# Kernel tuning notes

Hardware: AMD Instinct MI355X
Metric: run time of the kernel (lower is better)

## Reference

```python
import jax, jax.numpy as jnp
import numpy as np

# Model dims (GatedAttentionLayer of Qwen3.5 ANE hybrid stack)
C = 2048      # hidden_size
H = 16        # num_attention_heads
HK = 4        # num_key_value_heads
D = 128       # head_dim
ROT = 32      # rotary_dim = head_dim * partial_rotary_factor (0.25)
S = 1024      # sequence length (prefill)
CTX = 1024    # kv cache context length
N_ATTN = 6    # number of full-attention layers -> kv_cache leading dim 2*N_ATTN
EPS = 1e-6
ROPE_THETA = 1e7


def _rotate_half(x):
    h = x.shape[-1] // 2
    return jnp.concatenate([-x[..., h:], x[..., :h]], axis=-1)


def _rms_norm(x, w, eps=EPS):
    # Qwen3.5 convention: stored weight is (w - 1), applied as (1 + weight)
    r = jax.lax.rsqrt(jnp.mean(x * x, axis=-1, keepdims=True) + eps)
    return x * r * (1.0 + w)


def setup_inputs() -> dict:
    key = jax.random.key(0)
    ks = jax.random.split(key, 6)
    hidden_states = jax.random.normal(ks[0], (1, C, 1, S), jnp.float32)
    q_proj_w = jax.random.normal(ks[1], (H * 2 * D, C), jnp.float32) * 0.02  # q + gate
    k_proj_w = jax.random.normal(ks[2], (HK * D, C), jnp.float32) * 0.02
    v_proj_w = jax.random.normal(ks[3], (HK * D, C), jnp.float32) * 0.02
    o_proj_w = jax.random.normal(ks[4], (C, H * D), jnp.float32) * 0.02
    q_norm_w = jnp.zeros((D,), jnp.float32)
    k_norm_w = jnp.zeros((D,), jnp.float32)
    kv_cache = jnp.zeros((2 * N_ATTN, HK, CTX, D), jnp.float32)
    position_ids = jnp.arange(S, dtype=jnp.int32)
    # causal mask: 0 on/below diagonal, -1e9 above
    causal_mask = jnp.where(
        jnp.arange(CTX)[None, :] <= jnp.arange(S)[:, None], 0.0, -1e9
    ).astype(jnp.float32)[None, None]  # [1,1,S,CTX]
    # RoPE tables over rotary_dim
    inv_freq = 1.0 / (ROPE_THETA ** (jnp.arange(0, ROT, 2, dtype=jnp.float32) / ROT))
    t = jnp.arange(CTX, dtype=jnp.float32)
    freqs = jnp.outer(t, inv_freq)          # [CTX, ROT//2]
    emb = jnp.concatenate([freqs, freqs], -1)  # [CTX, ROT]
    cos_cached = jnp.cos(emb)
    sin_cached = jnp.sin(emb)
    return dict(hidden_states=hidden_states, q_proj_w=q_proj_w, k_proj_w=k_proj_w,
                v_proj_w=v_proj_w, o_proj_w=o_proj_w, q_norm_w=q_norm_w,
                k_norm_w=k_norm_w, kv_cache=kv_cache, causal_mask=causal_mask,
                position_ids=position_ids, cos_cached=cos_cached,
                sin_cached=sin_cached, attn_layer_idx=0)


def reference(hidden_states, q_proj_w, k_proj_w, v_proj_w, o_proj_w,
              q_norm_w, k_norm_w, kv_cache, causal_mask, position_ids,
              cos_cached, sin_cached, attn_layer_idx):
    x = hidden_states[0, :, 0, :]                     # [C, S]
    q_raw = q_proj_w @ x                              # [H*2D, S]  (1x1 Conv2d == GEMM)
    qg = q_raw.reshape(H, 2 * D, S)
    q = jnp.transpose(qg[:, :D, :], (0, 2, 1))        # [H, S, D]
    gate = jnp.transpose(qg[:, D:, :], (0, 2, 1))     # [H, S, D]
    k = jnp.transpose((k_proj_w @ x).reshape(HK, D, S), (0, 2, 1))  # [HK, S, D]
    v = jnp.transpose((v_proj_w @ x).reshape(HK, D, S), (0, 2, 1))  # [HK, S, D]

    q = _rms_norm(q, q_norm_w)
    k = _rms_norm(k, k_norm_w)

    cos = cos_cached[position_ids]   # [S, ROT]
    sin = sin_cached[position_ids]

    def rope(t):
        rot, pas = t[..., :ROT], t[..., ROT:]
        rot = rot * cos + _rotate_half(rot) * sin
        return jnp.concatenate([rot, pas], axis=-1)

    q, k = rope(q), rope(k)

    # prefill cache write at pos_start = position_ids[0]
    k_idx = 2 * attn_layer_idx
    v_idx = k_idx + 1
    pos_start = position_ids[0]
    kv_cache = jax.lax.dynamic_update_slice(kv_cache, k[None], (k_idx, 0, pos_start, 0))
    kv_cache = jax.lax.dynamic_update_slice(kv_cache, v[None], (v_idx, 0, pos_start, 0))

    g = H // HK  # GQA repeat (expand+reshape == contiguous repeat)
    k_full = jnp.repeat(kv_cache[k_idx], g, axis=0)   # [H, CTX, D]
    v_full = jnp.repeat(kv_cache[v_idx], g, axis=0)   # [H, CTX, D]

    scale = D ** -0.5
    attn = jnp.einsum('hsd,htd->hst', q, k_full) * scale + causal_mask[0]
    attn = jax.nn.softmax(attn, axis=-1)
    out = jnp.einsum('hst,htd->hsd', attn, v_full)    # [H, S, D]
    out = out * jax.nn.sigmoid(gate)
    out = jnp.transpose(out, (0, 2, 1)).reshape(H * D, S)
    output = (o_proj_w @ out)[None, :, None, :]       # [1, C, 1, S]
    return output
```

## Files before the change

### kernel.cpp

```cpp
#include <hip/hip_runtime.h>
#include <cstdint>

#define S_LEN 1024
#define C_DIM 2048
#define NH    16
#define NHK   4
#define HD    128
#define ROT   32
#define SCALE 0.08838834764831845f

typedef __bf16 bf16x8 __attribute__((ext_vector_type(8)));
typedef float floatx4 __attribute__((ext_vector_type(4)));
typedef float floatx16 __attribute__((ext_vector_type(16)));
typedef unsigned short ushortx8 __attribute__((ext_vector_type(8)));

__device__ __forceinline__ unsigned short f2bf(float f) {
  union { float f; uint32_t u; } x; x.f = f;
  uint32_t r = (x.u + 0x7fffu + ((x.u >> 16) & 1u)) >> 16;
  return (unsigned short)r;
}
__device__ __forceinline__ float bf2f(unsigned short v) {
  union { uint32_t u; float f; } x; x.u = (uint32_t)v << 16; return x.f;
}

__device__ __forceinline__ void async_copy16(const unsigned short* g, unsigned short* l) {
  __builtin_amdgcn_global_load_lds(
      (const __attribute__((address_space(1))) void*)g,
      (__attribute__((address_space(3))) void*)l,
      16, 0, 0);
}

__device__ __forceinline__ void bar_lds_only() {
  asm volatile("s_waitcnt lgkmcnt(0)" ::: "memory");
  __builtin_amdgcn_s_barrier();
}

__device__ __forceinline__ int swz8(int row) { return (row ^ (row >> 3)) & 7; }

__global__ __launch_bounds__(256)
void prep_kernel(const float* __restrict__ qw, const float* __restrict__ kw,
                 const float* __restrict__ vw, const float* __restrict__ ow,
                 unsigned short* __restrict__ wout,
                 const float* __restrict__ x, unsigned short* __restrict__ xT) {
  __shared__ float t[32][33];
  int bid = blockIdx.x;
  if (bid < 14336) {
    const int NQ = 4096 * 2048 / 4, NK = 512 * 2048 / 4, NV = 512 * 2048 / 4;
    int i = bid * 256 + threadIdx.x;
    const float* src; int j;
    if (i < NQ) { src = qw; j = i; }
    else if (i < NQ + NK) { src = kw; j = i - NQ; }
    else if (i < NQ + NK + NV) { src = vw; j = i - NQ - NK; }
    else { src = ow; j = i - NQ - NK - NV; }
    float4 v = ((const float4*)src)[j];
    ushort4 o;
    o.x = f2bf(v.x); o.y = f2bf(v.y); o.z = f2bf(v.z); o.w = f2bf(v.w);
    ((ushort4*)wout)[i] = o;
  } else {
    int b2 = bid - 14336;
    int st = b2 & 31, ct = b2 >> 5;
    int c = threadIdx.x & 31, rq = threadIdx.x >> 5;
#pragma unroll
    for (int i = 0; i < 4; ++i) {
      int r = rq + i * 8;
      t[r][c] = x[(size_t)(ct * 32 + r) * S_LEN + st * 32 + c];
    }
    __syncthreads();
#pragma unroll
    for (int i = 0; i < 4; ++i) {
      int r = rq + i * 8;
      xT[(size_t)(st * 32 + r) * C_DIM + ct * 32 + c] = f2bf(t[c][r]);
    }
  }
}

__device__ __forceinline__ void norm_rope_epi512(
    floatx16& acc, float (*pp)[32],
    const float* __restrict__ w, const int* __restrict__ pos_ids,
    const float* __restrict__ cosc, const float* __restrict__ sinc,
    unsigned short* __restrict__ outp,
    int wave, int lane, int wm, int scol0) {
  int l31 = lane & 31, half = lane >> 5;
  float s = 0.f;
#pragma unroll
  for (int reg = 0; reg < 16; ++reg) { float v = acc[reg]; s += v * v; }
  s += __shfl_xor(s, 32);
  if (half == 0) pp[wave][l31] = s;
  __syncthreads();
  int gb = wave & 4;
  float tot = pp[gb][l31] + pp[gb + 1][l31] + pp[gb + 2][l31] + pp[gb + 3][l31];
  float rn = rsqrtf(tot * (1.0f / 128.0f) + 1e-6f);
  int scol = scol0 + l31;
  int pos = pos_ids[scol];
  bool rope = (wm == 0);
#pragma unroll
  for (int g = 0; g < 4; ++g) {
    int dbase = wm + half * 4 + g * 8;
    ushort4 o;
#pragma unroll
    for (int rr = 0; rr < 4; ++rr) {
      int reg = g * 4 + rr;
      int d = dbase + rr;
      float v = acc[reg] * rn * (1.0f + w[d]);
      if (rope) {
        float cv = cosc[pos * ROT + d], sv = sinc[pos * ROT + d];
        int d2 = (d < 16) ? d + 16 : d - 16;
        float pv = acc[reg ^ 8] * rn * (1.0f + w[d2]);
        v = v * cv + ((d < 16) ? -pv : pv) * sv;
      }
      ((unsigned short*)&o)[rr] = f2bf(v);
    }
    *(ushort4*)&outp[(size_t)scol * HD + dbase] = o;
  }
}

#define GEMM512_CORE(EXTRA_LB)                                                     \
  int tid = threadIdx.x, wave = tid >> 6, lane = tid & 63;                         \
  int l31 = lane & 31, half = lane >> 5;                                           \
  int wm = (wave & 3) * 32, wn = (wave >> 2) * 32;                                 \
  int m0 = blockIdx.x * 128, n0 = blockIdx.y * 64;                                 \
  int r8 = tid >> 3, c8 = tid & 7;                                                 \
  int arow1 = r8 + 64;                                                             \
  int apos0 = c8 ^ swz8(r8), apos1 = c8 ^ swz8(arow1), bpos = apos0;               \
  int aswz = swz8(wm + l31), bswz = swz8(wn + l31);                                \
  const unsigned short* Ag = A + (size_t)m0 * C_DIM;                               \
  const unsigned short* Bg = BT + (size_t)n0 * C_DIM;                              \
  floatx16 acc = (floatx16)0.f;                                                    \
  ushortx8 rA0, rA1, rB;                                                           \
  rA0 = *(const ushortx8*)(Ag + (size_t)r8 * C_DIM + c8 * 8);                      \
  rA1 = *(const ushortx8*)(Ag + (size_t)arow1 * C_DIM + c8 * 8);                   \
  rB  = *(const ushortx8*)(Bg + (size_t)r8 * C_DIM + c8 * 8);                      \
  *(ushortx8*)&Asm[0][r8 * 64 + apos0 * 8] = rA0;                                  \
  *(ushortx8*)&Asm[0][arow1 * 64 + apos1 * 8] = rA1;                               \
  *(ushortx8*)&Bsm[0][r8 * 64 + bpos * 8] = rB;                                    \
  bar_lds_only();                                                                  \
  for (int t = 0; t < 32; ++t) {                                                   \
    int b = t & 1;                                                                 \
    if (t < 31) {                                                                  \
      int kt = (t + 1) * 64;                                                       \
      rA0 = *(const ushortx8*)(Ag + (size_t)r8 * C_DIM + kt + c8 * 8);             \
      rA1 = *(const ushortx8*)(Ag + (size_t)arow1 * C_DIM + kt + c8 * 8);          \
      rB  = *(const ushortx8*)(Bg + (size_t)r8 * C_DIM + kt + c8 * 8);             \
    }                                                                              \
    _Pragma("unroll")                                                              \
    for (int kb = 0; kb < 4; ++kb) {                                               \
      int ca = (((kb << 1) | half) ^ aswz) << 3;                                   \
      int cb = (((kb << 1) | half) ^ bswz) << 3;                                   \
      bf16x8 av = *(const bf16x8*)&Asm[b][(wm + l31) * 64 + ca];                   \
      bf16x8 bv = *(const bf16x8*)&Bsm[b][(wn + l31) * 64 + cb];                   \
      acc = __builtin_amdgcn_mfma_f32_32x32x16_bf16(av, bv, acc, 0, 0, 0);         \
    }                                                                              \
    if (t < 31) {                                                                  \
      *(ushortx8*)&Asm[b ^ 1][r8 * 64 + apos0 * 8] = rA0;                          \
      *(ushortx8*)&Asm[b ^ 1][arow1 * 64 + apos1 * 8] = rA1;                       \
      *(ushortx8*)&Bsm[b ^ 1][r8 * 64 + bpos * 8] = rB;                            \
    }                                                                              \
    bar_lds_only();                                                                \
  }

__global__ __launch_bounds__(512, 6)
void gemm_qkv_fused(const unsigned short* __restrict__ A,
                    const unsigned short* __restrict__ BT,
                    const float* __restrict__ qw, const float* __restrict__ kw,
                    const int* __restrict__ pos_ids,
                    const float* __restrict__ cosc, const float* __restrict__ sinc,
                    unsigned short* __restrict__ qb, unsigned short* __restrict__ kbuf,
                    unsigned short* __restrict__ vTb, unsigned short* __restrict__ sgb) {
  __shared__ unsigned short Asm[2][128 * 64];
  __shared__ unsigned short Bsm[2][64 * 64];
  __shared__ float pp[8][32];
  GEMM512_CORE()

  int scol0 = n0 + wn;
  int ty = blockIdx.x;
  if (ty < 32) {
    int h = ty >> 1;
    if ((ty & 1) == 0) {
      norm_rope_epi512(acc, pp, qw, pos_ids, cosc, sinc,
                       qb + (size_t)h * S_LEN * HD, wave, lane, wm, scol0);
    } else {
      int scol = scol0 + l31;
#pragma unroll
      for (int g = 0; g < 4; ++g) {
        int dbase = wm + half * 4 + g * 8;
        ushort4 o;
#pragma unroll
        for (int rr = 0; rr < 4; ++rr)
          ((unsigned short*)&o)[rr] = f2bf(1.0f / (1.0f + __expf(-acc[g * 4 + rr])));
        *(ushort4*)&sgb[((size_t)h * S_LEN + scol) * HD + dbase] = o;
      }
    }
  } else if (ty < 36) {
    int hk = ty - 32;
    norm_rope_epi512(acc, pp, kw, pos_ids, cosc, sinc,
                     kbuf + (size_t)hk * S_LEN * HD, wave, lane, wm, scol0);
  } else {
    int hk = ty - 36;
#pragma unroll
    for (int reg = 0; reg < 16; ++reg) {
      int d = wm + (reg & 3) + 8 * (reg >> 2) + 4 * half;
      vTb[(size_t)hk * HD * S_LEN + (size_t)d * S_LEN + scol0 + l31] = f2bf(acc[reg]);
    }
  }
}

__global__ __launch_bounds__(512, 6)
void gemm_oproj(const unsigned short* __restrict__ A,
                const unsigned short* __restrict__ BT,
                float* __restrict__ C) {
  __shared__ unsigned short Asm[2][128 * 64];
  __shared__ unsigned short Bsm[2][64 * 64];
  GEMM512_CORE()

#pragma unroll
  for (int reg = 0; reg < 16; ++reg) {
    int row = m0 + wm + (reg & 3) + 8 * (reg >> 2) + 4 * half;
    C[(size_t)row * S_LEN + n0 + wn + l31] = acc[reg];
  }
}

__global__ __launch_bounds__(256)
void attn_kernel(const unsigned short* __restrict__ qb,
                 const unsigned short* __restrict__ kbuf,
                 const unsigned short* __restrict__ vTb,
                 float* __restrict__ pm, float* __restrict__ pl,
                 float* __restrict__ pO0, float* __restrict__ pO1) {
  __shared__ __align__(16) unsigned short Ks[64 * 128];
  __shared__ __align__(16) unsigned short Vs[128 * 64];
  __shared__ __align__(16) unsigned short Ps[4][16][72];
  int h = blockIdx.x, qt = blockIdx.y, ch = blockIdx.z;
  int t0 = ch * 4;
  if (t0 > qt) return;
  int t1 = min(qt, t0 + 3);
  int s0 = qt * 64;
  int hk = h >> 2;
  int tid = threadIdx.x, wave = tid >> 6, lane = tid & 63;
  int l16 = lane & 15, quad = lane >> 4;
  int lsw = l16 & 7;

  const unsigned short* qg = qb + ((size_t)(h * S_LEN + s0 + wave * 16 + l16)) * HD;
  bf16x8 qfr[4];
#pragma unroll
  for (int kb = 0; kb < 4; ++kb)
    qfr[kb] = *(const bf16x8*)(qg + kb * 32 + quad * 8);

  float m_r[4], l_r[4];
#pragma unroll
  for (int r = 0; r < 4; ++r) { m_r[r] = -1e30f; l_r[r] = 0.f; }
  floatx4 acc_o[8];
#pragma unroll
  for (int i = 0; i < 8; ++i) acc_o[i] = (floatx4)0.f;
  int srow_base = s0 + wave * 16 + quad * 4;

  const unsigned short* kg0 = kbuf + (size_t)hk * S_LEN * HD;
  const unsigned short* vg0 = vTb + (size_t)hk * HD * S_LEN;

  int kr4 = lane >> 4, kc16 = lane & 15;
  int vr8 = lane >> 3, vc8 = lane & 7;

  for (int t = t0; t <= t1; ++t) {
    int jt = t * 64;
#pragma unroll
    for (int i = 0; i < 4; ++i) {
      int rbase = wave * 16 + i * 4;
      int row = rbase + kr4;
      int cs = kc16 ^ (row & 7);
      async_copy16(kg0 + (size_t)(jt + row) * HD + cs * 8, Ks + rbase * 128);
    }
#pragma unroll
    for (int i = 0; i < 4; ++i) {
      int rbase = wave * 32 + i * 8;
      int row = rbase + vr8;
      int cs = vc8 ^ (row & 7);
      async_copy16(vg0 + (size_t)row * S_LEN + jt + cs * 8, Vs + rbase * 64);
    }
    __syncthreads();

    floatx4 acc_s[4];
#pragma unroll
    for (int ni = 0; ni < 4; ++ni) acc_s[ni] = (floatx4)0.f;
#pragma unroll
    for (int kb = 0; kb < 4; ++kb) {
#pragma unroll
      for (int ni = 0; ni < 4; ++ni) {
        int cl = (kb * 4 + quad) ^ lsw;
        bf16x8 bk = *(const bf16x8*)&Ks[(ni * 16 + l16) * 128 + cl * 8];
        acc_s[ni] = __builtin_amdgcn_mfma_f32_16x16x32_bf16(qfr[kb], bk, acc_s[ni], 0, 0, 0);
      }
    }

    bool diag = (t == qt);
    float alpha[4];
#pragma unroll
    for (int r = 0; r < 4; ++r) {
      float scv[4];
      float mx = -1e30f;
#pragma unroll
      for (int ni = 0; ni < 4; ++ni) {
        float sv = acc_s[ni][r] * SCALE;
        if (diag) {
          int jg = jt + ni * 16 + l16;
          if (jg > srow_base + r) sv = -1e30f;
        }
        scv[ni] = sv;
        mx = fmaxf(mx, sv);
      }
#pragma unroll
      for (int off = 8; off; off >>= 1) mx = fmaxf(mx, __shfl_xor(mx, off, 16));
      float mnew = fmaxf(m_r[r], mx);
      float psv = 0.f;
#pragma unroll
      for (int ni = 0; ni < 4; ++ni) {
        float pv = (scv[ni] > -1e29f) ? __expf(scv[ni] - mnew) : 0.f;
        Ps[wave][quad * 4 + r][ni * 16 + l16] = f2bf(pv);
        psv += pv;
      }
#pragma unroll
      for (int off = 8; off; off >>= 1) psv += __shfl_xor(psv, off, 16);
      alpha[r] = __expf(m_r[r] - mnew);
      m_r[r] = mnew;
      l_r[r] = l_r[r] * alpha[r] + psv;
    }
#pragma unroll
    for (int i = 0; i < 8; ++i)
#pragma unroll
      for (int r = 0; r < 4; ++r) acc_o[i][r] *= alpha[r];
    __threadfence_block();

#pragma unroll
    for (int kb2 = 0; kb2 < 2; ++kb2) {
      bf16x8 ap = *(const bf16x8*)&Ps[wave][l16][kb2 * 32 + quad * 8];
#pragma unroll
      for (int ni2 = 0; ni2 < 8; ++ni2) {
        int cl = (kb2 * 4 + quad) ^ lsw;
        bf16x8 bv = *(const bf16x8*)&Vs[(ni2 * 16 + l16) * 64 + cl * 8];
        acc_o[ni2] = __builtin_amdgcn_mfma_f32_16x16x32_bf16(ap, bv, acc_o[ni2], 0, 0, 0);
      }
    }
    __syncthreads();
  }

  size_t pmbase = ((size_t)(h * 16 + qt) * 4 + ch) * 64;
  float* pOp = (ch < 2) ? pO0 + ((size_t)(h * 16 + qt) * 2 + ch) * 8192
                        : pO1 + ((size_t)(h * 16 + qt) * 2 + (ch - 2)) * 8192;
#pragma unroll
  for (int r = 0; r < 4; ++r) {
    int rrow = wave * 16 + quad * 4 + r;
    if (l16 == 0) { pm[pmbase + rrow] = m_r[r]; pl[pmbase + rrow] = l_r[r]; }
#pragma unroll
    for (int ni2 = 0; ni2 < 8; ++ni2)
      pOp[rrow * 128 + ni2 * 16 + l16] = acc_o[ni2][r];
  }
}

__global__ __launch_bounds__(256)
void attn_merge(const float* __restrict__ pm, const float* __restrict__ pl,
                const float* __restrict__ pO0, const float* __restrict__ pO1,
                const unsigned short* __restrict__ sgb,
                unsigned short* __restrict__ outT) {
  int h = blockIdx.x, qt = blockIdx.y;
  int vc = (qt >> 2) + 1;
  size_t base = (size_t)(h * 16 + qt) * 4;
  int lane32 = threadIdx.x & 31, rb = threadIdx.x >> 5;
  int d = lane32 * 4;
#pragma unroll
  for (int rr = 0; rr < 8; ++rr) {
    int row = rr * 8 + rb;
    float M = -1e30f;
    for (int c = 0; c < vc; ++c) M = fmaxf(M, pm[(base + c) * 64 + row]);
    float L = 0.f;
    floatx4 acc = (floatx4)0.f;
    for (int c = 0; c < vc; ++c) {
      float w = __expf(pm[(base + c) * 64 + row] - M);
      L += w * pl[(base + c) * 64 + row];
      const float* Op = (c < 2) ? pO0 + ((size_t)(h * 16 + qt) * 2 + c) * 8192
                                : pO1 + ((size_t)(h * 16 + qt) * 2 + (c - 2)) * 8192;
      floatx4 o = *(const floatx4*)&Op[row * 128 + d];
#pragma unroll
      for (int j = 0; j < 4; ++j) acc[j] += w * o[j];
    }
    float inv = 1.0f / L;
    int s = qt * 64 + row;
    ushort4 sg4 = *(const ushort4*)&sgb[((size_t)h * S_LEN + s) * HD + d];
    ushort4 out4;
#pragma unroll
    for (int j = 0; j < 4; ++j)
      ((unsigned short*)&out4)[j] = f2bf(acc[j] * inv * bf2f(((unsigned short*)&sg4)[j]));
    *(ushort4*)&outT[(size_t)s * (NH * HD) + h * HD + d] = out4;
  }
}

extern "C" void kernel_launch(void* const* d_in, const int* in_sizes, int n_in,
                              void* d_out, int out_size, void* d_ws, size_t ws_size,
                              hipStream_t stream) {
  const float* hs       = (const float*)d_in[0];
  const float* q_proj_w = (const float*)d_in[1];
  const float* k_proj_w = (const float*)d_in[2];
  const float* v_proj_w = (const float*)d_in[3];
  const float* o_proj_w = (const float*)d_in[4];
  const float* q_norm_w = (const float*)d_in[5];
  const float* k_norm_w = (const float*)d_in[6];
  const int*   pos_ids  = (const int*)d_in[9];
  const float* cos_c    = (const float*)d_in[10];
  const float* sin_c    = (const float*)d_in[11];
  float* out = (float*)d_out;

  char* ws = (char*)d_ws;
  unsigned short* wqkv = (unsigned short*)(ws + 0);
  unsigned short* wo   = (unsigned short*)(ws + 20971520);
  unsigned short* xT   = (unsigned short*)(ws + 29360128);
  unsigned short* qb   = (unsigned short*)(ws + 33554432);
  unsigned short* kbuf = (unsigned short*)(ws + 37748736);
  unsigned short* vTb  = (unsigned short*)(ws + 38797312);
  unsigned short* sgb  = (unsigned short*)(ws + 39845888);
  unsigned short* aoT  = (unsigned short*)(ws + 44040192);
  float*          pO0  = (float*)(ws + 0);
  float*          pO1  = (float*)(ws + 48234496);
  float*          pm   = (float*)(ws + 65011712);
  float*          pl   = (float*)(ws + 65273856);

  prep_kernel<<<14336 + 2048, 256, 0, stream>>>(q_proj_w, k_proj_w, v_proj_w, o_proj_w,
                                                wqkv, hs, xT);
  gemm_qkv_fused<<<dim3(40, 16), 512, 0, stream>>>(wqkv, xT, q_norm_w, k_norm_w,
                                                   pos_ids, cos_c, sin_c,
                                                   qb, kbuf, vTb, sgb);
  attn_kernel<<<dim3(16, 16, 4), 256, 0, stream>>>(qb, kbuf, vTb, pm, pl, pO0, pO1);
  attn_merge<<<dim3(16, 16), 256, 0, stream>>>(pm, pl, pO0, pO1, sgb, aoT);
  gemm_oproj<<<dim3(16, 16), 512, 0, stream>>>(wo, aoT, out);
}
```

Baseline: 241.8 us.

## Rewrite QKV GEMM with 4 waves, direct global-to-LDS async loads

The fused QKV projection GEMM moves from 8 waves (512 threads) holding one 32x32 accumulator each to 4 waves holding two accumulators, so each A fragment read from LDS feeds two MFMAs. Tile staging now uses global_load_lds async copies into double-buffered LDS, gated by vmcnt waits, instead of staging through registers and LDS stores. The RMS-norm/RoPE epilogue is reworked to handle two column blocks per wave. The intent is to cut LDS traffic and register staging overhead and overlap loads with compute, at the cost of fewer waves per block for hiding latency.

Result: faster. 232.7 us (-3.8%).

```diff
diff --git a/kernel.cpp b/kernel.cpp
--- a/kernel.cpp
+++ b/kernel.cpp
@@ -29,6 +29,8 @@
       (__attribute__((address_space(3))) void*)l,
       16, 0, 0);
 }
+
+#define WAIT_VM(N) asm volatile("s_waitcnt vmcnt(" #N ")" ::: "memory")
 
 __device__ __forceinline__ void bar_lds_only() {
   asm volatile("s_waitcnt lgkmcnt(0)" ::: "memory");
@@ -74,43 +76,145 @@
   }
 }
 
-__device__ __forceinline__ void norm_rope_epi512(
-    floatx16& acc, float (*pp)[32],
+__device__ __forceinline__ void norm_rope_epi4(
+    floatx16 (&acc)[2], float (*pp)[64],
     const float* __restrict__ w, const int* __restrict__ pos_ids,
     const float* __restrict__ cosc, const float* __restrict__ sinc,
     unsigned short* __restrict__ outp,
     int wave, int lane, int wm, int scol0) {
   int l31 = lane & 31, half = lane >> 5;
-  float s = 0.f;
-#pragma unroll
-  for (int reg = 0; reg < 16; ++reg) { float v = acc[reg]; s += v * v; }
-  s += __shfl_xor(s, 32);
-  if (half == 0) pp[wave][l31] = s;
+#pragma unroll
+  for (int ni = 0; ni < 2; ++ni) {
+    float s = 0.f;
+#pragma unroll
+    for (int reg = 0; reg < 16; ++reg) { float v = acc[ni][reg]; s += v * v; }
+    s += __shfl_xor(s, 32);
+    if (half == 0) pp[wave][ni * 32 + l31] = s;
+  }
   __syncthreads();
-  int gb = wave & 4;
-  float tot = pp[gb][l31] + pp[gb + 1][l31] + pp[gb + 2][l31] + pp[gb + 3][l31];
-  float rn = rsqrtf(tot * (1.0f / 128.0f) + 1e-6f);
-  int scol = scol0 + l31;
-  int pos = pos_ids[scol];
-  bool rope = (wm == 0);
-#pragma unroll
-  for (int g = 0; g < 4; ++g) {
-    int dbase = wm + half * 4 + g * 8;
-    ushort4 o;
-#pragma unroll
-    for (int rr = 0; rr < 4; ++rr) {
-      int reg = g * 4 + rr;
-      int d = dbase + rr;
-      float v = acc[reg] * rn * (1.0f + w[d]);
-      if (rope) {
-        float cv = cosc[pos * ROT + d], sv = sinc[pos * ROT + d];
-        int d2 = (d < 16) ? d + 16 : d - 16;
-        float pv = acc[reg ^ 8] * rn * (1.0f + w[d2]);
-        v = v * cv + ((d < 16) ? -pv : pv) * sv;
-      }
-      ((unsigned short*)&o)[rr] = f2bf(v);
-    }
-    *(ushort4*)&outp[(size_t)scol * HD + dbase] = o;
+#pragma unroll
+  for (int ni = 0; ni < 2; ++ni) {
+    int ci = ni * 32 + l31;
+    float tot = pp[0][ci] + pp[1][ci] + pp[2][ci] + pp[3][ci];
+    float rn = rsqrtf(tot * (1.0f / 128.0f) + 1e-6f);
+    int scol = scol0 + ni * 32 + l31;
+    int pos = pos_ids[scol];
+    bool rope = (wm == 0);
+#pragma unroll
+    for (int g = 0; g < 4; ++g) {
+      int dbase = wm + half * 4 + g * 8;
+      ushort4 o;
+#pragma unroll
+      for (int rr = 0; rr < 4; ++rr) {
+        int reg = g * 4 + rr;
+        int d = dbase + rr;
+        float v = acc[ni][reg] * rn * (1.0f + w[d]);
+        if (rope) {
+          float cv = cosc[pos * ROT + d], sv = sinc[pos * ROT + d];
+          int d2 = (d < 16) ? d + 16 : d - 16;
+          float pv = acc[ni][reg ^ 8] * rn * (1.0f + w[d2]);
+          v = v * cv + ((d < 16) ? -pv : pv) * sv;
+        }
+        ((unsigned short*)&o)[rr] = f2bf(v);
+      }
+      *(ushort4*)&outp[(size_t)scol * HD + dbase] = o;
+    }
+  }
+}
+
+#define STAGE_QKV4(B_, KT)                                                     \
+  { _Pragma("unroll")                                                          \
+    for (int i = 0; i < 4; ++i) {                                              \
+      int row = wm + i * 8 + sr;                                               \
+      async_copy16(Ag + (size_t)row * C_DIM + (KT) + (sc ^ swz8(row)) * 8,     \
+                   &Asm[B_][(wm + i * 8) * 64]);                               \
+    }                                                                          \
+    _Pragma("unroll")                                                          \
+    for (int i = 0; i < 2; ++i) {                                              \
+      int row = wave * 16 + i * 8 + sr;                                        \
+      async_copy16(Bg + (size_t)row * C_DIM + (KT) + (sc ^ swz8(row)) * 8,     \
+                   &Bsm[B_][(wave * 16 + i * 8) * 64]);                        \
+    } }
+
+__global__ __launch_bounds__(256, 3)
+void gemm_qkv_fused(const unsigned short* __restrict__ A,
+                    const unsigned short* __restrict__ BT,
+                    const float* __restrict__ qw, const float* __restrict__ kw,
+                    const int* __restrict__ pos_ids,
+                    const float* __restrict__ cosc, const float* __restrict__ sinc,
+                    unsigned short* __restrict__ qb, unsigned short* __restrict__ kbuf,
+                    unsigned short* __restrict__ vTb, unsigned short* __restrict__ sgb) {
+  __shared__ unsigned short Asm[2][128 * 64];
+  __shared__ unsigned short Bsm[2][64 * 64];
+  __shared__ float pp[4][64];
+  int tid = threadIdx.x, wave = tid >> 6, lane = tid & 63;
+  int l31 = lane & 31, half = lane >> 5;
+  int wm = wave * 32;
+  int m0 = blockIdx.x * 128, n0 = blockIdx.y * 64;
+  int sr = lane >> 3, sc = lane & 7;
+  const unsigned short* Ag = A + (size_t)m0 * C_DIM;
+  const unsigned short* Bg = BT + (size_t)n0 * C_DIM;
+  int aswz = swz8(wm + l31);
+  int bswz0 = swz8(l31), bswz1 = swz8(32 + l31);
+  floatx16 acc[2];
+  acc[0] = (floatx16)0.f; acc[1] = (floatx16)0.f;
+
+  STAGE_QKV4(0, 0)
+  STAGE_QKV4(1, 64)
+
+  for (int t = 0; t < 32; ++t) {
+    int b = t & 1;
+    if (t < 31) { WAIT_VM(6); } else { WAIT_VM(0); }
+    __builtin_amdgcn_s_barrier();
+#pragma unroll
+    for (int kb = 0; kb < 4; ++kb) {
+      int c2 = (kb << 1) | half;
+      bf16x8 av  = *(const bf16x8*)&Asm[b][(wm + l31) * 64 + ((c2 ^ aswz) << 3)];
+      bf16x8 b0v = *(const bf16x8*)&Bsm[b][l31 * 64 + ((c2 ^ bswz0) << 3)];
+      bf16x8 b1v = *(const bf16x8*)&Bsm[b][(32 + l31) * 64 + ((c2 ^ bswz1) << 3)];
+      acc[0] = __builtin_amdgcn_mfma_f32_32x32x16_bf16(av, b0v, acc[0], 0, 0, 0);
+      acc[1] = __builtin_amdgcn_mfma_f32_32x32x16_bf16(av, b1v, acc[1], 0, 0, 0);
+    }
+    bar_lds_only();
+    if (t < 30) STAGE_QKV4(b, (t + 2) * 64)
+  }
+
+  int scol0 = n0;
+  int ty = blockIdx.x;
+  if (ty < 32) {
+    int h = ty >> 1;
+    if ((ty & 1) == 0) {
+      norm_rope_epi4(acc, pp, qw, pos_ids, cosc, sinc,
+                     qb + (size_t)h * S_LEN * HD, wave, lane, wm, scol0);
+    } else {
+#pragma unroll
+      for (int ni = 0; ni < 2; ++ni) {
+        int scol = scol0 + ni * 32 + l31;
+#pragma unroll
+        for (int g = 0; g < 4; ++g) {
+          int dbase = wm + half * 4 + g * 8;
+          ushort4 o;
+#pragma unroll
+          for (int rr = 0; rr < 4; ++rr)
+            ((unsigned short*)&o)[rr] = f2bf(1.0f / (1.0f + __expf(-acc[ni][g * 4 + rr])));
+          *(ushort4*)&sgb[((size_t)h * S_LEN + scol) * HD + dbase] = o;
+        }
+      }
+    }
+  } else if (ty < 36) {
+    int hk = ty - 32;
+    norm_rope_epi4(acc, pp, kw, pos_ids, cosc, sinc,
+                   kbuf + (size_t)hk * S_LEN * HD, wave, lane, wm, scol0);
+  } else {
+    int hk = ty - 36;
+#pragma unroll
+    for (int ni = 0; ni < 2; ++ni)
+#pragma unroll
+      for (int reg = 0; reg < 16; ++reg) {
+        int d = wm + (reg & 3) + 8 * (reg >> 2) + 4 * half;
+        vTb[(size_t)hk * HD * S_LEN + (size_t)d * S_LEN + scol0 + ni * 32 + l31] =
+            f2bf(acc[ni][reg]);
+      }
   }
 }
 
@@ -159,52 +263,6 @@
   }
 
 __global__ __launch_bounds__(512, 6)
-void gemm_qkv_fused(const unsigned short* __restrict__ A,
-                    const unsigned short* __restrict__ BT,
-                    const float* __restrict__ qw, const float* __restrict__ kw,
-                    const int* __restrict__ pos_ids,
-                    const float* __restrict__ cosc, const float* __restrict__ sinc,
-                    unsigned short* __restrict__ qb, unsigned short* __restrict__ kbuf,
-                    unsigned short* __restrict__ vTb, unsigned short* __restrict__ sgb) {
-  __shared__ unsigned short Asm[2][128 * 64];
-  __shared__ unsigned short Bsm[2][64 * 64];
-  __shared__ float pp[8][32];
-  GEMM512_CORE()
-
-  int scol0 = n0 + wn;
-  int ty = blockIdx.x;
-  if (ty < 32) {
-    int h = ty >> 1;
-    if ((ty & 1) == 0) {
-      norm_rope_epi512(acc, pp, qw, pos_ids, cosc, sinc,
-                       qb + (size_t)h * S_LEN * HD, wave, lane, wm, scol0);
-    } else {
-      int scol = scol0 + l31;
-#pragma unroll
-      for (int g = 0; g < 4; ++g) {
-        int dbase = wm + half * 4 + g * 8;
-        ushort4 o;
-#pragma unroll
-        for (int rr = 0; rr < 4; ++rr)
-          ((unsigned short*)&o)[rr] = f2bf(1.0f / (1.0f + __expf(-acc[g * 4 + rr])));
-        *(ushort4*)&sgb[((size_t)h * S_LEN + scol) * HD + dbase] = o;
-      }
-    }
-  } else if (ty < 36) {
-    int hk = ty - 32;
-    norm_rope_epi512(acc, pp, kw, pos_ids, cosc, sinc,
-                     kbuf + (size_t)hk * S_LEN * HD, wave, lane, wm, scol0);
-  } else {
-    int hk = ty - 36;
-#pragma unroll
-    for (int reg = 0; reg < 16; ++reg) {
-      int d = wm + (reg & 3) + 8 * (reg >> 2) + 4 * half;
-      vTb[(size_t)hk * HD * S_LEN + (size_t)d * S_LEN + scol0 + l31] = f2bf(acc[reg]);
-    }
-  }
-}
-
-__global__ __launch_bounds__(512, 6)
 void gemm_oproj(const unsigned short* __restrict__ A,
                 const unsigned short* __restrict__ BT,
                 float* __restrict__ C) {
@@ -421,7 +479,7 @@
 
   prep_kernel<<<14336 + 2048, 256, 0, stream>>>(q_proj_w, k_proj_w, v_proj_w, o_proj_w,
                                                 wqkv, hs, xT);
-  gemm_qkv_fused<<<dim3(40, 16), 512, 0, stream>>>(wqkv, xT, q_norm_w, k_norm_w,
+  gemm_qkv_fused<<<dim3(40, 16), 256, 0, stream>>>(wqkv, xT, q_norm_w, k_norm_w,
                                                    pos_ids, cos_c, sin_c,
                                                    qb, kbuf, vTb, sgb);
   attn_kernel<<<dim3(16, 16, 4), 256, 0, stream>>>(qb, kbuf, vTb, pm, pl, pO0, pO1);
```
